# Optimization experiments

Measured on AMD Instinct MI355X. Metric: run time of the kernel, lower is better.

## Reference

```python
import jax, jax.numpy as jnp
import numpy as np

BN_EPS = 1e-5
N_OUT, D_OUT = 64, 128


def setup_inputs() -> dict:
    key = jax.random.key(0)
    k1, k2, k3, k4 = jax.random.split(key, 4)
    B, N_in, D_in, K = 512, 64, 128, 4
    x = jax.random.normal(k1, (B, N_in, D_in), dtype=jnp.float32)
    # block-sparse weights: one (D_in x D_out) block per (output-row, active-input-row) pair
    W = jax.random.normal(k2, (N_OUT, K, D_in, D_OUT), dtype=jnp.float32) * (1.0 / np.sqrt(K * D_in))
    bias = jax.random.normal(k3, (N_OUT, D_OUT), dtype=jnp.float32) * 0.02
    gamma = jnp.ones((N_OUT * D_OUT,), dtype=jnp.float32)
    beta = jnp.zeros((N_OUT * D_OUT,), dtype=jnp.float32)
    idx = jax.random.randint(k4, (N_OUT, K), 0, N_in, dtype=jnp.int32)
    return {"x": x, "W": W, "bias": bias, "gamma": gamma, "beta": beta, "idx": idx}


def reference(x, W, bias, gamma, beta, idx):
    B = x.shape[0]
    # structured-sparse linear: gather active input rows, per-block matmul
    xg = x[:, idx, :]                                   # [B, N_out, K, D_in]
    y = jnp.einsum('bokd,okde->boe', xg, W) + bias      # [B, N_out, D_out]
    # BatchNorm1d (training-mode batch statistics) on flattened features
    yf = y.reshape(B, -1)                               # [B, N_out*D_out]
    mean = jnp.mean(yf, axis=0)
    var = jnp.mean(jnp.square(yf - mean), axis=0)       # biased variance, as in torch BN
    yn = (yf - mean) * jax.lax.rsqrt(var + BN_EPS) * gamma + beta
    # Swish: z * sigmoid(z)
    out = yn * jax.nn.sigmoid(yn)
    return out.reshape(B, N_OUT, D_OUT)
```

## Files before the change

### kernel.cpp

```cpp
#include <hip/hip_runtime.h>


typedef __attribute__((ext_vector_type(8))) __bf16 bf16x8;
typedef __attribute__((ext_vector_type(4))) __bf16 bf16x4;
typedef __attribute__((ext_vector_type(4))) float  f32x4;

#define B_SZ   512
#define N_IN   64
#define D_IN   128
#define FEAT   8192
#define LDA    40
#define LDT    130

__global__ __launch_bounds__(256, 2)
void prep_w_kernel(const float* __restrict__ W, __bf16* __restrict__ Wt2)
{
    __shared__ __bf16 T[128 * LDT];
    const int o    = blockIdx.x >> 2;
    const int kidx = blockIdx.x & 3;
    const int tid  = threadIdx.x;

#pragma unroll
    for (int it = 0; it < 16; ++it) {
        const int lin = it * 1024 + tid * 4;
        const int d   = lin >> 7;
        const int e   = lin & 127;
        f32x4 v = *(const f32x4*)(W + (((o * 4 + kidx) * 128 + d) * 128 + e));
        bf16x4 b;
        b[0] = (__bf16)v[0]; b[1] = (__bf16)v[1];
        b[2] = (__bf16)v[2]; b[3] = (__bf16)v[3];
        *(bf16x4*)&T[d * LDT + e] = b;
    }
    __syncthreads();

#pragma unroll
    for (int it = 0; it < 8; ++it) {
        const int task = it * 256 + tid;
        const int e    = task >> 4;
        const int dc   = task & 15;
        bf16x8 v;
#pragma unroll
        for (int j = 0; j < 8; ++j) v[j] = T[(dc * 8 + j) * LDT + e];
        const int kk  = kidx * 4 + (dc >> 2);
        const int kin = (dc & 3) * 8;
        *(bf16x8*)(Wt2 + (((o * 16 + kk) * 128 + e) * 32 + kin)) = v;
    }
}

__global__ __launch_bounds__(256, 2)
void gemm_stats_kernel(const float* __restrict__ x, const __bf16* __restrict__ Wt2,
                       const float* __restrict__ bias, const int* __restrict__ idxp,
                       __bf16* __restrict__ y, float* __restrict__ psum,
                       float* __restrict__ psq)
{
    __shared__ __bf16 Alds[2][64 * LDA];

    const int bx   = blockIdx.x;
    const int o    = bx >> 3;
    const int bt   = bx & 7;
    const int b0   = bt * 64;
    const int tid  = threadIdx.x;
    const int wave = tid >> 6;
    const int lane = tid & 63;
    const int lam  = lane & 15;
    const int quad = lane >> 4;
    const int nbase = wave * 32;

    int rsel[4];
#pragma unroll
    for (int k = 0; k < 4; ++k) rsel[k] = idxp[o * 4 + k];

    const f32x4 zero4 = {0.f, 0.f, 0.f, 0.f};
    f32x4 acc[4][2];
#pragma unroll
    for (int mi = 0; mi < 4; ++mi)
#pragma unroll
        for (int ni = 0; ni < 2; ++ni) acc[mi][ni] = zero4;

    const int m_a = tid >> 2;
    const int ca  = (tid & 3) * 8;

    const __bf16* bptr = Wt2 + ((size_t)(o * 16) * 128 + nbase + lam) * 32 + quad * 8;

    f32x4 xv0, xv1;
    {
        const int r = rsel[0];
        const float* xa = x + (((b0 + m_a) * N_IN + r) * D_IN + ca);
        xv0 = *(const f32x4*)(xa + 0);
        xv1 = *(const f32x4*)(xa + 4);
    }

    for (int kk = 0; kk < 16; ++kk) {
        bf16x8 p;
        p[0] = (__bf16)xv0[0]; p[1] = (__bf16)xv0[1];
        p[2] = (__bf16)xv0[2]; p[3] = (__bf16)xv0[3];
        p[4] = (__bf16)xv1[0]; p[5] = (__bf16)xv1[1];
        p[6] = (__bf16)xv1[2]; p[7] = (__bf16)xv1[3];
        const int buf = kk & 1;
        *(bf16x8*)&Alds[buf][m_a * LDA + ca] = p;
        __syncthreads();

        if (kk < 15) {
            const int kn = kk + 1;
            const int r  = rsel[kn >> 2];
            const int d0 = (kn & 3) * 32;
            const float* xa = x + (((b0 + m_a) * N_IN + r) * D_IN + d0 + ca);
            xv0 = *(const f32x4*)(xa + 0);
            xv1 = *(const f32x4*)(xa + 4);
        }

        bf16x8 bfv[2];
#pragma unroll
        for (int ni = 0; ni < 2; ++ni)
            bfv[ni] = *(const bf16x8*)(bptr + ((size_t)kk * 128 + ni * 16) * 32);

        bf16x8 af[4];
#pragma unroll
        for (int mi = 0; mi < 4; ++mi)
            af[mi] = *(const bf16x8*)&Alds[buf][(mi * 16 + lam) * LDA + quad * 8];

#pragma unroll
        for (int mi = 0; mi < 4; ++mi)
#pragma unroll
            for (int ni = 0; ni < 2; ++ni)
                acc[mi][ni] = __builtin_amdgcn_mfma_f32_16x16x32_bf16(
                    af[mi], bfv[ni], acc[mi][ni], 0, 0, 0);
    }

    float bvals[2];
#pragma unroll
    for (int ni = 0; ni < 2; ++ni)
        bvals[ni] = bias[o * 128 + nbase + ni * 16 + lam];

#pragma unroll
    for (int mi = 0; mi < 4; ++mi)
#pragma unroll
        for (int ni = 0; ni < 2; ++ni)
#pragma unroll
            for (int rr = 0; rr < 4; ++rr) acc[mi][ni][rr] += bvals[ni];

#pragma unroll
    for (int mi = 0; mi < 4; ++mi) {
        const int mrow = b0 + mi * 16 + quad * 4;
#pragma unroll
        for (int ni = 0; ni < 2; ++ni) {
            const int col = o * 128 + nbase + ni * 16 + lam;
#pragma unroll
            for (int rr = 0; rr < 4; ++rr)
                y[(mrow + rr) * FEAT + col] = (__bf16)acc[mi][ni][rr];
        }
    }

#pragma unroll
    for (int ni = 0; ni < 2; ++ni) {
        float s = 0.f, q = 0.f;
#pragma unroll
        for (int mi = 0; mi < 4; ++mi)
#pragma unroll
            for (int rr = 0; rr < 4; ++rr) {
                const float v = acc[mi][ni][rr];
                s += v; q += v * v;
            }
        s += __shfl_xor(s, 16); s += __shfl_xor(s, 32);
        q += __shfl_xor(q, 16); q += __shfl_xor(q, 32);
        if (quad == 0) {
            const int e = nbase + ni * 16 + lam;
            psum[(o * 8 + bt) * 128 + e] = s;
            psq [(o * 8 + bt) * 128 + e] = q;
        }
    }
}

__global__ __launch_bounds__(256, 4)
void norm_silu_kernel(const __bf16* __restrict__ y, const float* __restrict__ psum,
                      const float* __restrict__ psq, const float* __restrict__ gamma,
                      const float* __restrict__ beta, float* __restrict__ out)
{
    __shared__ float sscale[128];
    __shared__ float sshift[128];
    const int o   = blockIdx.x >> 3;
    const int bc  = blockIdx.x & 7;
    const int tid = threadIdx.x;

    if (tid < 128) {
        float s = 0.f, q = 0.f;
#pragma unroll
        for (int sl = 0; sl < 8; ++sl) {
            s += psum[(o * 8 + sl) * 128 + tid];
            q += psq [(o * 8 + sl) * 128 + tid];
        }
        const float mean = s * (1.0f / 512.0f);
        const float var  = q * (1.0f / 512.0f) - mean * mean;
        const float rstd = rsqrtf(var + 1e-5f);
        const float sc   = rstd * gamma[o * 128 + tid];
        sscale[tid] = sc;
        sshift[tid] = beta[o * 128 + tid] - mean * sc;
    }
    __syncthreads();

#pragma unroll
    for (int it = 0; it < 4; ++it) {
        const int lin = it * 2048 + tid * 8;
        const int bl  = lin >> 7;
        const int e   = lin & 127;
        const int g   = (bc * 64 + bl) * FEAT + o * 128 + e;
        bf16x8 y8 = *(const bf16x8*)&y[g];
        f32x4 ov0, ov1;
#pragma unroll
        for (int j = 0; j < 4; ++j) {
            const float v  = (float)y8[j];
            const float xn = v * sscale[e + j] + sshift[e + j];
            ov0[j] = xn / (1.0f + __expf(-xn));
        }
#pragma unroll
        for (int j = 0; j < 4; ++j) {
            const float v  = (float)y8[4 + j];
            const float xn = v * sscale[e + 4 + j] + sshift[e + 4 + j];
            ov1[j] = xn / (1.0f + __expf(-xn));
        }
        *(f32x4*)&out[g]     = ov0;
        *(f32x4*)&out[g + 4] = ov1;
    }
}

extern "C" void kernel_launch(void* const* d_in, const int* in_sizes, int n_in,
                              void* d_out, int out_size, void* d_ws, size_t ws_size,
                              hipStream_t stream)
{
    const float* x     = (const float*)d_in[0];
    const float* W     = (const float*)d_in[1];
    const float* bias  = (const float*)d_in[2];
    const float* gamma = (const float*)d_in[3];
    const float* beta  = (const float*)d_in[4];
    const int*   idx   = (const int*)d_in[5];
    float* out = (float*)d_out;

    __bf16* y    = (__bf16*)d_ws;
    __bf16* Wt2  = y + (size_t)B_SZ * FEAT;
    float*  psum = (float*)(Wt2 + (size_t)64 * 512 * 128);
    float*  psq  = psum + 64 * 8 * 128;

    prep_w_kernel<<<dim3(256), dim3(256), 0, stream>>>(W, Wt2);
    gemm_stats_kernel<<<dim3(512), dim3(256), 0, stream>>>(x, Wt2, bias, idx, y, psum, psq);
    norm_silu_kernel<<<dim3(512), dim3(256), 0, stream>>>(y, psum, psq, gamma, beta, out);
}
```

Measured before the change: 109.5 us.

## Fuse GEMM, batch-norm and SiLU via cooperative grid sync

Merges the GEMM+stats kernel and the normalize+SiLU kernel into one cooperative kernel. Blocks write partial sums, synchronize across the whole grid, then apply BN and Swish directly from the accumulator registers. This drops the bf16 intermediate y round-trip through global memory and one launch. The cost is a grid-wide barrier and output stores that are scattered per-lane scalars rather than vectorized. It also depends on all 512 blocks being co-resident. The prep kernel's LDS padding also changes from 130 to 132.

```diff
diff --git a/kernel.cpp b/kernel.cpp
--- a/kernel.cpp
+++ b/kernel.cpp
@@ -1,4 +1,7 @@
 #include <hip/hip_runtime.h>
+#include <hip/hip_cooperative_groups.h>
+
+namespace cg = cooperative_groups;
 
 
 typedef __attribute__((ext_vector_type(8))) __bf16 bf16x8;
@@ -10,7 +13,7 @@
 #define D_IN   128
 #define FEAT   8192
 #define LDA    40
-#define LDT    130
+#define LDT    132
 
 __global__ __launch_bounds__(256, 2)
 void prep_w_kernel(const float* __restrict__ W, __bf16* __restrict__ Wt2)
@@ -48,12 +51,15 @@
 }
 
 __global__ __launch_bounds__(256, 2)
-void gemm_stats_kernel(const float* __restrict__ x, const __bf16* __restrict__ Wt2,
-                       const float* __restrict__ bias, const int* __restrict__ idxp,
-                       __bf16* __restrict__ y, float* __restrict__ psum,
-                       float* __restrict__ psq)
+void gemm_bn_silu_kernel(const float* __restrict__ x, const __bf16* __restrict__ Wt2,
+                         const float* __restrict__ bias, const int* __restrict__ idxp,
+                         const float* __restrict__ gamma, const float* __restrict__ beta,
+                         float* __restrict__ out, float* __restrict__ psum,
+                         float* __restrict__ psq)
 {
     __shared__ __bf16 Alds[2][64 * LDA];
+    __shared__ float sscale[128];
+    __shared__ float sshift[128];
 
     const int bx   = blockIdx.x;
     const int o    = bx >> 3;
@@ -140,18 +146,6 @@
             for (int rr = 0; rr < 4; ++rr) acc[mi][ni][rr] += bvals[ni];
 
 #pragma unroll
-    for (int mi = 0; mi < 4; ++mi) {
-        const int mrow = b0 + mi * 16 + quad * 4;
-#pragma unroll
-        for (int ni = 0; ni < 2; ++ni) {
-            const int col = o * 128 + nbase + ni * 16 + lam;
-#pragma unroll
-            for (int rr = 0; rr < 4; ++rr)
-                y[(mrow + rr) * FEAT + col] = (__bf16)acc[mi][ni][rr];
-        }
-    }
-
-#pragma unroll
     for (int ni = 0; ni < 2; ++ni) {
         float s = 0.f, q = 0.f;
 #pragma unroll
@@ -169,18 +163,9 @@
             psq [(o * 8 + bt) * 128 + e] = q;
         }
     }
-}
-
-__global__ __launch_bounds__(256, 4)
-void norm_silu_kernel(const __bf16* __restrict__ y, const float* __restrict__ psum,
-                      const float* __restrict__ psq, const float* __restrict__ gamma,
-                      const float* __restrict__ beta, float* __restrict__ out)
-{
-    __shared__ float sscale[128];
-    __shared__ float sshift[128];
-    const int o   = blockIdx.x >> 3;
-    const int bc  = blockIdx.x & 7;
-    const int tid = threadIdx.x;
+
+    __threadfence();
+    cg::this_grid().sync();
 
     if (tid < 128) {
         float s = 0.f, q = 0.f;
@@ -199,27 +184,20 @@
     __syncthreads();
 
 #pragma unroll
-    for (int it = 0; it < 4; ++it) {
-        const int lin = it * 2048 + tid * 8;
-        const int bl  = lin >> 7;
-        const int e   = lin & 127;
-        const int g   = (bc * 64 + bl) * FEAT + o * 128 + e;
-        bf16x8 y8 = *(const bf16x8*)&y[g];
-        f32x4 ov0, ov1;
-#pragma unroll
-        for (int j = 0; j < 4; ++j) {
-            const float v  = (float)y8[j];
-            const float xn = v * sscale[e + j] + sshift[e + j];
-            ov0[j] = xn / (1.0f + __expf(-xn));
-        }
-#pragma unroll
-        for (int j = 0; j < 4; ++j) {
-            const float v  = (float)y8[4 + j];
-            const float xn = v * sscale[e + 4 + j] + sshift[e + 4 + j];
-            ov1[j] = xn / (1.0f + __expf(-xn));
-        }
-        *(f32x4*)&out[g]     = ov0;
-        *(f32x4*)&out[g + 4] = ov1;
+    for (int mi = 0; mi < 4; ++mi) {
+        const int mrow = b0 + mi * 16 + quad * 4;
+#pragma unroll
+        for (int ni = 0; ni < 2; ++ni) {
+            const int cl = nbase + ni * 16 + lam;
+            const float sc = sscale[cl];
+            const float sh = sshift[cl];
+#pragma unroll
+            for (int rr = 0; rr < 4; ++rr) {
+                const float xn = acc[mi][ni][rr] * sc + sh;
+                out[(size_t)(mrow + rr) * FEAT + o * 128 + cl] =
+                    xn / (1.0f + __expf(-xn));
+            }
+        }
     }
 }
 
@@ -235,12 +213,15 @@
     const int*   idx   = (const int*)d_in[5];
     float* out = (float*)d_out;
 
-    __bf16* y    = (__bf16*)d_ws;
-    __bf16* Wt2  = y + (size_t)B_SZ * FEAT;
+    __bf16* Wt2  = (__bf16*)d_ws;
     float*  psum = (float*)(Wt2 + (size_t)64 * 512 * 128);
     float*  psq  = psum + 64 * 8 * 128;
 
     prep_w_kernel<<<dim3(256), dim3(256), 0, stream>>>(W, Wt2);
-    gemm_stats_kernel<<<dim3(512), dim3(256), 0, stream>>>(x, Wt2, bias, idx, y, psum, psq);
-    norm_silu_kernel<<<dim3(512), dim3(256), 0, stream>>>(y, psum, psq, gamma, beta, out);
+
+    void* args[] = { (void*)&x, (void*)&Wt2, (void*)&bias, (void*)&idx,
+                     (void*)&gamma, (void*)&beta, (void*)&out,
+                     (void*)&psum, (void*)&psq };
+    hipLaunchCooperativeKernel((const void*)gemm_bn_silu_kernel,
+                               dim3(512), dim3(256), args, 0, stream);
 }
```

Measured after the change: 203.3 us. 1.86x slower.
